# Kernel optimization log

Measured on AMD Instinct MI355X. Metric: run time of the kernel, lower is better.

## Reference

```python
import jax, jax.numpy as jnp
import numpy as np

B, N, D, H = 2048, 200, 128, 8

def setup_inputs() -> dict:
    key = jax.random.key(0)
    k1, k2, k3, k4, k5, k6 = jax.random.split(key, 6)
    return {
        "item_embedding": jax.random.normal(k1, (B, N, D), dtype=jnp.float32),
        "query_embedding": jax.random.normal(k2, (B, D), dtype=jnp.float32),
        "mask": jax.random.randint(k3, (B, N, 1), 0, 2).astype(bool),
        "Wq": jax.random.normal(k4, (D * H, D), dtype=jnp.float32) * 0.05,
        "bq": jax.random.normal(k5, (D * H,), dtype=jnp.float32) * 0.05,
        "Wr": jax.random.normal(k6, (1, H), dtype=jnp.float32) * 0.5,
    }

def reference(item_embedding, query_embedding, mask, Wq, bq, Wr):
    b = query_embedding.shape[0]
    # query projection + tanh, reshape to (B, D, H)
    pq = jnp.tanh(query_embedding @ Wq.T + bq).reshape(b, D, H)
    # batched dot: (B,N,D) @ (B,D,H) -> (B,N,H)
    dotted = jnp.einsum('bnd,bdh->bnh', item_embedding, pq)
    # head reduce: (B,N,H) @ (H,1) -> (B,N,1)
    reduced = dotted @ Wr.T
    scores = reduced - jnp.max(reduced, axis=1, keepdims=True)
    att = jnp.exp(scores) * mask
    denom = jnp.sum(att, axis=1, keepdims=True)
    weight = att / jnp.where(denom < 1e-7, denom + 1.0, denom)
    # weighted sum pooling -> (B, D)
    return jnp.sum(weight * item_embedding, axis=1)
```

## Files before the change

### kernel.cpp

```cpp
#include <hip/hip_runtime.h>

#define BB 2048
#define NN 200
#define DD 128
#define HH 8

typedef float f4v __attribute__((ext_vector_type(4)));

__global__ __launch_bounds__(256) void proj_kernel(
    const float* __restrict__ q,
    const float* __restrict__ Wq,
    const float* __restrict__ bq,
    const float* __restrict__ Wr,
    float* __restrict__ v)
{
    __shared__ float wq_s[32][257];
    const int t  = threadIdx.x;
    const int jc = blockIdx.x;
    const int b0 = blockIdx.y * 16;
    const int j  = jc * 256 + t;

    float acc[16];
#pragma unroll
    for (int i = 0; i < 16; ++i) acc[i] = 0.f;

    for (int kt = 0; kt < 4; ++kt) {
        __syncthreads();
#pragma unroll
        for (int i = 0; i < 8; ++i) {
            int idx = t + 256 * i;
            int jj  = idx >> 3;
            int kf  = idx & 7;
            const float4 w4 = *(const float4*)(Wq + (size_t)(jc*256 + jj)*128 + kt*32 + kf*4);
            wq_s[kf*4+0][jj] = w4.x;
            wq_s[kf*4+1][jj] = w4.y;
            wq_s[kf*4+2][jj] = w4.z;
            wq_s[kf*4+3][jj] = w4.w;
        }
        __syncthreads();

        float wreg[32];
#pragma unroll
        for (int k = 0; k < 32; ++k) wreg[k] = wq_s[k][t];

#pragma unroll
        for (int bb = 0; bb < 16; ++bb) {
            const float* qrow = q + (size_t)(b0 + bb)*128 + kt*32;
            float s = 0.f;
#pragma unroll
            for (int k = 0; k < 32; ++k) s = fmaf(qrow[k], wreg[k], s);
            acc[bb] += s;
        }
    }

    const float bqj = bq[j];
    const float wrh = Wr[j & 7];
    const int   d   = j >> 3;
#pragma unroll
    for (int bb = 0; bb < 16; ++bb) {
        float p = tanhf(acc[bb] + bqj) * wrh;
        p += __shfl_xor(p, 1);
        p += __shfl_xor(p, 2);
        p += __shfl_xor(p, 4);
        if ((t & 7) == 0) v[(size_t)(b0 + bb)*128 + d] = p;
    }
}

__global__ __launch_bounds__(512, 8) void attn_kernel(
    const float* __restrict__ item,
    const int*   __restrict__ mask,
    const float* __restrict__ v,
    float* __restrict__ out)
{
    __shared__ float item_s[72][132];
    __shared__ float red_s[72];
    __shared__ float w_s[72];

    const int t    = threadIdx.x;
    const int b    = blockIdx.x;
    const int seg  = t & 31;
    const int half = t >> 5;
    const int l64  = t & 63;
    const int d    = t & 127;
    const int p    = t >> 7;

    const f4v vreg = *(const f4v*)(v + (size_t)b*128 + seg*4);
    const float* itemb = item + (size_t)b * (NN * 128);

    float m = -3e38f, lsum = 0.f, o_part = 0.f;

    f4v pre[5];
#pragma unroll
    for (int i = 0; i < 5; ++i) {
        const int row = half + 16*i;
        pre[i] = (f4v)0.f;
        if (row < 64)
            pre[i] = __builtin_nontemporal_load(
                (const f4v*)(itemb + (size_t)row*128 + seg*4));
    }

    for (int c = 0; c < 3; ++c) {
        const int base = c * 64;
        const int rows = (c == 2) ? 72 : 64;
        __syncthreads();

#pragma unroll
        for (int i = 0; i < 5; ++i) {
            const int row = half + 16*i;
            if (row < rows) {
                const f4v f = pre[i];
                float pp = f[0]*vreg[0] + f[1]*vreg[1] + f[2]*vreg[2] + f[3]*vreg[3];
#pragma unroll
                for (int off = 16; off >= 1; off >>= 1)
                    pp += __shfl_xor(pp, off);
                *(f4v*)(&item_s[row][seg*4]) = f;
                if (seg == 0) red_s[row] = pp;
            }
        }

        if (c < 2) {
            const int nbase = (c + 1) * 64;
            const int nrows = (c == 1) ? 72 : 64;
#pragma unroll
            for (int i = 0; i < 5; ++i) {
                const int row = half + 16*i;
                pre[i] = (f4v)0.f;
                if (row < nrows)
                    pre[i] = __builtin_nontemporal_load(
                        (const f4v*)(itemb + (size_t)(nbase + row)*128 + seg*4));
            }
        }
        __syncthreads();

        float mv = red_s[l64];
        if (c == 2 && l64 < 8) mv = fmaxf(mv, red_s[64 + l64]);
#pragma unroll
        for (int off = 32; off >= 1; off >>= 1)
            mv = fmaxf(mv, __shfl_xor(mv, off));
        const float new_m = fmaxf(m, mv);
        const float alpha = __expf(m - new_m);
        m = new_m;

        if (t < rows) {
            const int mk = mask[(size_t)b * NN + base + t];
            w_s[t] = mk ? __expf(red_s[t] - new_m) : 0.f;
        }
        __syncthreads();

        float sv = w_s[l64];
        if (c == 2 && l64 < 8) sv += w_s[64 + l64];
#pragma unroll
        for (int off = 32; off >= 1; off >>= 1)
            sv += __shfl_xor(sv, off);
        lsum = lsum * alpha + sv;

        const int rpp = rows >> 2;
        float acc = 0.f;
#pragma unroll
        for (int nn = 0; nn < 18; ++nn)
            if (nn < rpp)
                acc = fmaf(w_s[p*rpp + nn], item_s[p*rpp + nn][d], acc);
        o_part = o_part * alpha + acc;
    }

    __syncthreads();
    item_s[p][d] = o_part;
    __syncthreads();
    if (t < 128) {
        const float tot   = item_s[0][t] + item_s[1][t] + item_s[2][t] + item_s[3][t];
        const float denom = (lsum < 1e-7f) ? (lsum + 1.f) : lsum;
        out[(size_t)b * 128 + t] = tot / denom;
    }
}

extern "C" void kernel_launch(void* const* d_in, const int* in_sizes, int n_in,
                              void* d_out, int out_size, void* d_ws, size_t ws_size,
                              hipStream_t stream) {
    const float* item = (const float*)d_in[0];
    const float* q    = (const float*)d_in[1];
    const int*   mask = (const int*)  d_in[2];
    const float* Wq   = (const float*)d_in[3];
    const float* bq   = (const float*)d_in[4];
    const float* Wr   = (const float*)d_in[5];
    float* out = (float*)d_out;
    float* v   = (float*)d_ws;

    proj_kernel<<<dim3(4, 128), 256, 0, stream>>>(q, Wq, bq, Wr, v);
    attn_kernel<<<dim3(BB), 512, 0, stream>>>(item, mask, v, out);
}
```

Measured before the change: 342.1 us.

## Keep item tiles in registers with per-wave online softmax partials

The attention kernel no longer stages item rows and scores in shared memory. Each wave computes its own max, sum and weighted accumulator over the rows it loaded, and a small shared array of (max, sum) pairs merges the results across waves. Mask values are prefetched along with the item rows, and the final 16 partial outputs are reduced through shared memory. This cuts LDS traffic and two barriers per chunk, at the cost of more exp evaluations and a 16-way final reduction.

```diff
diff --git a/kernel.cpp b/kernel.cpp
--- a/kernel.cpp
+++ b/kernel.cpp
@@ -72,51 +72,67 @@
     const float* __restrict__ v,
     float* __restrict__ out)
 {
-    __shared__ float item_s[72][132];
-    __shared__ float red_s[72];
-    __shared__ float w_s[72];
+    __shared__ float2 ml_s[3][16];
+    __shared__ __align__(16) float stage[16][132];
 
     const int t    = threadIdx.x;
     const int b    = blockIdx.x;
     const int seg  = t & 31;
     const int half = t >> 5;
-    const int l64  = t & 63;
-    const int d    = t & 127;
-    const int p    = t >> 7;
 
     const f4v vreg = *(const f4v*)(v + (size_t)b*128 + seg*4);
     const float* itemb = item + (size_t)b * (NN * 128);
+    const int*   maskb = mask + (size_t)b * NN;
 
-    float m = -3e38f, lsum = 0.f, o_part = 0.f;
+    float m = -3e38f, lsum = 0.f;
+    f4v o4 = (f4v)0.f;
 
     f4v pre[5];
+    int mk[5];
 #pragma unroll
     for (int i = 0; i < 5; ++i) {
         const int row = half + 16*i;
-        pre[i] = (f4v)0.f;
-        if (row < 64)
+        pre[i] = (f4v)0.f; mk[i] = 0;
+        if (row < 64) {
             pre[i] = __builtin_nontemporal_load(
                 (const f4v*)(itemb + (size_t)row*128 + seg*4));
+            mk[i] = maskb[row];
+        }
     }
 
     for (int c = 0; c < 3; ++c) {
-        const int base = c * 64;
         const int rows = (c == 2) ? 72 : 64;
-        __syncthreads();
 
+        float pp[5];
 #pragma unroll
         for (int i = 0; i < 5; ++i) {
-            const int row = half + 16*i;
-            if (row < rows) {
-                const f4v f = pre[i];
-                float pp = f[0]*vreg[0] + f[1]*vreg[1] + f[2]*vreg[2] + f[3]*vreg[3];
+            const f4v f = pre[i];
+            float s = f[0]*vreg[0] + f[1]*vreg[1] + f[2]*vreg[2] + f[3]*vreg[3];
 #pragma unroll
-                for (int off = 16; off >= 1; off >>= 1)
-                    pp += __shfl_xor(pp, off);
-                *(f4v*)(&item_s[row][seg*4]) = f;
-                if (seg == 0) red_s[row] = pp;
+            for (int off = 16; off >= 1; off >>= 1)
+                s += __shfl_xor(s, off);
+            pp[i] = s;
+        }
+
+        float mh = -3e38f;
+#pragma unroll
+        for (int i = 0; i < 5; ++i)
+            if (half + 16*i < rows) mh = fmaxf(mh, pp[i]);
+
+        float lh = 0.f;
+        f4v oacc = (f4v)0.f;
+#pragma unroll
+        for (int i = 0; i < 5; ++i) {
+            if (half + 16*i < rows) {
+                const float w = mk[i] ? __expf(pp[i] - mh) : 0.f;
+                lh += w;
+                oacc[0] = fmaf(w, pre[i][0], oacc[0]);
+                oacc[1] = fmaf(w, pre[i][1], oacc[1]);
+                oacc[2] = fmaf(w, pre[i][2], oacc[2]);
+                oacc[3] = fmaf(w, pre[i][3], oacc[3]);
             }
         }
+        if (seg == 0) ml_s[c][half] = make_float2(mh, lh);
 
         if (c < 2) {
             const int nbase = (c + 1) * 64;
@@ -124,50 +140,43 @@
 #pragma unroll
             for (int i = 0; i < 5; ++i) {
                 const int row = half + 16*i;
-                pre[i] = (f4v)0.f;
-                if (row < nrows)
+                pre[i] = (f4v)0.f; mk[i] = 0;
+                if (row < nrows) {
                     pre[i] = __builtin_nontemporal_load(
                         (const f4v*)(itemb + (size_t)(nbase + row)*128 + seg*4));
+                    mk[i] = maskb[nbase + row];
+                }
             }
         }
         __syncthreads();
 
-        float mv = red_s[l64];
-        if (c == 2 && l64 < 8) mv = fmaxf(mv, red_s[64 + l64]);
+        float mc = mh;
 #pragma unroll
-        for (int off = 32; off >= 1; off >>= 1)
-            mv = fmaxf(mv, __shfl_xor(mv, off));
-        const float new_m = fmaxf(m, mv);
-        const float alpha = __expf(m - new_m);
-        m = new_m;
-
-        if (t < rows) {
-            const int mk = mask[(size_t)b * NN + base + t];
-            w_s[t] = mk ? __expf(red_s[t] - new_m) : 0.f;
+        for (int h = 0; h < 16; ++h)
+            mc = fmaxf(mc, ml_s[c][h].x);
+        const float m_new = fmaxf(m, mc);
+        const float alpha = __expf(m - m_new);
+        float lc = 0.f;
+#pragma unroll
+        for (int h = 0; h < 16; ++h) {
+            const float2 ml = ml_s[c][h];
+            lc += ml.y * __expf(ml.x - m_new);
         }
-        __syncthreads();
-
-        float sv = w_s[l64];
-        if (c == 2 && l64 < 8) sv += w_s[64 + l64];
-#pragma unroll
-        for (int off = 32; off >= 1; off >>= 1)
-            sv += __shfl_xor(sv, off);
-        lsum = lsum * alpha + sv;
-
-        const int rpp = rows >> 2;
-        float acc = 0.f;
-#pragma unroll
-        for (int nn = 0; nn < 18; ++nn)
-            if (nn < rpp)
-                acc = fmaf(w_s[p*rpp + nn], item_s[p*rpp + nn][d], acc);
-        o_part = o_part * alpha + acc;
+        lsum = lsum * alpha + lc;
+        const float beta = __expf(mh - m_new);
+        o4[0] = o4[0] * alpha + oacc[0] * beta;
+        o4[1] = o4[1] * alpha + oacc[1] * beta;
+        o4[2] = o4[2] * alpha + oacc[2] * beta;
+        o4[3] = o4[3] * alpha + oacc[3] * beta;
+        m = m_new;
     }
 
-    __syncthreads();
-    item_s[p][d] = o_part;
+    *(f4v*)(&stage[half][seg*4]) = o4;
     __syncthreads();
     if (t < 128) {
-        const float tot   = item_s[0][t] + item_s[1][t] + item_s[2][t] + item_s[3][t];
+        float tot = 0.f;
+#pragma unroll
+        for (int h = 0; h < 16; ++h) tot += stage[h][t];
         const float denom = (lsum < 1e-7f) ? (lsum + 1.f) : lsum;
         out[(size_t)b * 128 + t] = tot / denom;
     }
```

Result: slower. 392.7 us (+14.8%).

## Keep per-wave online softmax state in registers, merge partials at the end

Applied to the files above, without the earlier changes.

Restructures the attention kernel so that each 32-lane row group keeps its own running max, sum and weighted output in registers, using the rows it already holds. This removes the shared-memory staging of item tiles and the three block barriers per chunk. The mask is preloaded into shared memory once, and the 16 partial states are merged with a log-sum-exp rescale in a final reduction. In exchange there are more exp calls per thread and a small serial merge at the end.

```diff
diff --git a/kernel.cpp b/kernel.cpp
--- a/kernel.cpp
+++ b/kernel.cpp
@@ -72,22 +72,19 @@
     const float* __restrict__ v,
     float* __restrict__ out)
 {
-    __shared__ float item_s[72][132];
-    __shared__ float red_s[72];
-    __shared__ float w_s[72];
+    __shared__ float  mask_s[NN];
+    __shared__ float2 ml_s[16];
+    __shared__ __align__(16) float stage[16][132];
 
     const int t    = threadIdx.x;
     const int b    = blockIdx.x;
     const int seg  = t & 31;
     const int half = t >> 5;
-    const int l64  = t & 63;
-    const int d    = t & 127;
-    const int p    = t >> 7;
 
     const f4v vreg = *(const f4v*)(v + (size_t)b*128 + seg*4);
     const float* itemb = item + (size_t)b * (NN * 128);
 
-    float m = -3e38f, lsum = 0.f, o_part = 0.f;
+    if (t < NN) mask_s[t] = mask[(size_t)b * NN + t] ? 1.f : 0.f;
 
     f4v pre[5];
 #pragma unroll
@@ -98,23 +95,46 @@
             pre[i] = __builtin_nontemporal_load(
                 (const f4v*)(itemb + (size_t)row*128 + seg*4));
     }
+    __syncthreads();
+
+    float mh = -3e38f, lh = 0.f;
+    f4v oh = (f4v)0.f;
 
     for (int c = 0; c < 3; ++c) {
         const int base = c * 64;
         const int rows = (c == 2) ? 72 : 64;
-        __syncthreads();
+
+        float pp[5];
+#pragma unroll
+        for (int i = 0; i < 5; ++i) {
+            const f4v f = pre[i];
+            float s = f[0]*vreg[0] + f[1]*vreg[1] + f[2]*vreg[2] + f[3]*vreg[3];
+#pragma unroll
+            for (int off = 16; off >= 1; off >>= 1)
+                s += __shfl_xor(s, off);
+            pp[i] = s;
+        }
+
+        float mn = mh;
+#pragma unroll
+        for (int i = 0; i < 5; ++i)
+            if (half + 16*i < rows) mn = fmaxf(mn, pp[i]);
+
+        const float alpha = __expf(mh - mn);
+        mh = mn;
+        lh *= alpha;
+        oh[0] *= alpha; oh[1] *= alpha; oh[2] *= alpha; oh[3] *= alpha;
 
 #pragma unroll
         for (int i = 0; i < 5; ++i) {
             const int row = half + 16*i;
             if (row < rows) {
-                const f4v f = pre[i];
-                float pp = f[0]*vreg[0] + f[1]*vreg[1] + f[2]*vreg[2] + f[3]*vreg[3];
-#pragma unroll
-                for (int off = 16; off >= 1; off >>= 1)
-                    pp += __shfl_xor(pp, off);
-                *(f4v*)(&item_s[row][seg*4]) = f;
-                if (seg == 0) red_s[row] = pp;
+                const float w = mask_s[base + row] * __expf(pp[i] - mn);
+                lh += w;
+                oh[0] = fmaf(w, pre[i][0], oh[0]);
+                oh[1] = fmaf(w, pre[i][1], oh[1]);
+                oh[2] = fmaf(w, pre[i][2], oh[2]);
+                oh[3] = fmaf(w, pre[i][3], oh[3]);
             }
         }
 
@@ -130,44 +150,23 @@
                         (const f4v*)(itemb + (size_t)(nbase + row)*128 + seg*4));
             }
         }
-        __syncthreads();
-
-        float mv = red_s[l64];
-        if (c == 2 && l64 < 8) mv = fmaxf(mv, red_s[64 + l64]);
-#pragma unroll
-        for (int off = 32; off >= 1; off >>= 1)
-            mv = fmaxf(mv, __shfl_xor(mv, off));
-        const float new_m = fmaxf(m, mv);
-        const float alpha = __expf(m - new_m);
-        m = new_m;
-
-        if (t < rows) {
-            const int mk = mask[(size_t)b * NN + base + t];
-            w_s[t] = mk ? __expf(red_s[t] - new_m) : 0.f;
-        }
-        __syncthreads();
-
-        float sv = w_s[l64];
-        if (c == 2 && l64 < 8) sv += w_s[64 + l64];
-#pragma unroll
-        for (int off = 32; off >= 1; off >>= 1)
-            sv += __shfl_xor(sv, off);
-        lsum = lsum * alpha + sv;
-
-        const int rpp = rows >> 2;
-        float acc = 0.f;
-#pragma unroll
-        for (int nn = 0; nn < 18; ++nn)
-            if (nn < rpp)
-                acc = fmaf(w_s[p*rpp + nn], item_s[p*rpp + nn][d], acc);
-        o_part = o_part * alpha + acc;
     }
 
+    if (seg == 0) ml_s[half] = make_float2(mh, lh);
+    *(f4v*)(&stage[half][seg*4]) = oh;
     __syncthreads();
-    item_s[p][d] = o_part;
-    __syncthreads();
+
     if (t < 128) {
-        const float tot   = item_s[0][t] + item_s[1][t] + item_s[2][t] + item_s[3][t];
+        float mg = -3e38f;
+#pragma unroll
+        for (int h = 0; h < 16; ++h) mg = fmaxf(mg, ml_s[h].x);
+        float lsum = 0.f, tot = 0.f;
+#pragma unroll
+        for (int h = 0; h < 16; ++h) {
+            const float sc = __expf(ml_s[h].x - mg);
+            lsum += ml_s[h].y * sc;
+            tot  = fmaf(stage[h][t], sc, tot);
+        }
         const float denom = (lsum < 1e-7f) ? (lsum + 1.f) : lsum;
         out[(size_t)b * 128 + t] = tot / denom;
     }
```

Measured after the change: 320.1 us. -6.4%, faster.
